# Optimization experiments

Measured on AMD Instinct MI355X. Metric: run time of the kernel, lower is better.

## Reference

```python
import jax, jax.numpy as jnp
from jax import lax
import numpy as np

HIDDEN = 256
UID_EMB, LOC_EMB, WD_EMB, HR_EMB = 64, 128, 16, 16
UID_NUM, LOC_NUM = 5000, 50000
S, L, C = 32, 32, 128   # steps, current-trace prefix length, candidates per step
HN, LH = 32, 64         # history traces, history trace length
EMB = UID_EMB + LOC_EMB + WD_EMB + HR_EMB  # 224


def setup_inputs() -> dict:
    key = jax.random.key(0)
    ks = jax.random.split(key, 20)
    def lin(k, o, i, s=0.05):
        return jax.random.normal(k, (o, i), jnp.float32) * s
    return {
        "uid": 7,
        "current_trace": jnp.stack([
            jax.random.randint(ks[0], (S, L), 0, LOC_NUM),
            jax.random.randint(ks[1], (S, L), 0, 7),
            jax.random.randint(ks[2], (S, L), 0, 24)], axis=-1),
        "history_trace": jnp.stack([
            jax.random.randint(ks[3], (HN, LH), 0, LOC_NUM),
            jax.random.randint(ks[4], (HN, LH), 0, 7),
            jax.random.randint(ks[5], (HN, LH), 0, 24)], axis=-1),
        "candidate_set": jax.random.randint(ks[6], (S, C), 0, LOC_NUM),
        "uid_emb": jax.random.normal(ks[7], (UID_NUM, UID_EMB), jnp.float32),
        "loc_emb": jax.random.normal(ks[8], (LOC_NUM, LOC_EMB), jnp.float32),
        "weekday_emb": jax.random.normal(ks[9], (7, WD_EMB), jnp.float32),
        "hour_emb": jax.random.normal(ks[10], (24, HR_EMB), jnp.float32),
        "W_ih": lin(ks[11], 3 * HIDDEN, EMB),
        "W_hh": lin(ks[12], 3 * HIDDEN, HIDDEN),
        "b_ih": jnp.zeros((3 * HIDDEN,), jnp.float32),
        "b_hh": jnp.zeros((3 * HIDDEN,), jnp.float32),
        "intra_w1": lin(ks[13], HIDDEN, HIDDEN),
        "intra_w2": lin(ks[14], HIDDEN, HIDDEN),
        "intra_out": lin(ks[15], 1, HIDDEN),
        "inter_w1": lin(ks[16], HIDDEN, HIDDEN),
        "inter_w2": lin(ks[17], HIDDEN, HIDDEN),
        "inter_out": lin(ks[18], 1, HIDDEN),
        "score_w": lin(ks[19], 1, HIDDEN),
    }


def _gru(x, W_ih, W_hh, b_ih, b_hh):
    # x: [B, T, D] -> all hidden states [B, T, H]; single-layer torch GRU equations
    B = x.shape[0]
    H = W_hh.shape[1]
    x_proj = x @ W_ih.T + b_ih  # [B, T, 3H], precomputed input projection
    def step(h, xp):
        gh = h @ W_hh.T + b_hh
        xr, xz, xn = jnp.split(xp, 3, axis=-1)
        hr, hz, hn = jnp.split(gh, 3, axis=-1)
        r = jax.nn.sigmoid(xr + hr)
        z = jax.nn.sigmoid(xz + hz)
        n = jnp.tanh(xn + r * hn)
        h_new = (1.0 - z) * n + z * h
        return h_new, h_new
    h0 = jnp.zeros((B, H), x.dtype)
    _, hs = lax.scan(step, h0, jnp.swapaxes(x_proj, 0, 1))
    return jnp.swapaxes(hs, 0, 1)


def _forward(uid, current_trace, history_trace, candidate_set,
             uid_emb, loc_emb, weekday_emb, hour_emb,
             W_ih, W_hh, b_ih, b_hh,
             intra_w1, intra_w2, intra_out,
             inter_w1, inter_w2, inter_out, score_w):
    def encode(trace):  # [B, T, 3] int -> [B, H]
        B, T, _ = trace.shape
        u = jnp.broadcast_to(uid_emb[uid][None, None, :], (B, T, UID_EMB))
        e = jnp.concatenate([u,
                             loc_emb[trace[:, :, 0]],
                             weekday_emb[trace[:, :, 1]],
                             hour_emb[trace[:, :, 2]]], axis=-1)
        hs = _gru(e, W_ih, W_hh, b_ih, b_hh)
        # intra-trajectory attention: query = last hidden state, key = all hidden states
        qh = jax.nn.relu(hs[:, -1, :] @ intra_w1.T)[:, None, :]
        kh = jax.nn.relu(hs @ intra_w2.T)
        a = (jnp.tanh(qh + kh) @ intra_out.T)[..., 0]  # [B, T]
        w = jax.nn.softmax(a, axis=1)
        return jnp.einsum('bt,bth->bh', w, hs)

    hist_hidden = encode(history_trace)  # [HN, H]

    S_, L_, _ = current_trace.shape
    C_ = candidate_set.shape[1]
    last_time = current_trace[:, -1, 1:3]  # [S, 2] weekday/hour of last observed point
    cand_point = jnp.concatenate(
        [candidate_set[..., None],
         jnp.broadcast_to(last_time[:, None, :], (S_, C_, 2))], axis=-1)  # [S, C, 3]
    cand_trace = jnp.concatenate(
        [jnp.broadcast_to(current_trace[:, None], (S_, C_, L_, 3)),
         cand_point[:, :, None, :]], axis=2)  # [S, C, L+1, 3]
    cand_hidden = encode(cand_trace.reshape(S_ * C_, L_ + 1, 3))  # [S*C, H]

    # inter-trajectory attention; history key is shared across all candidates
    qh = jax.nn.relu(cand_hidden @ inter_w1.T)      # [S*C, H]
    kh = jax.nn.relu(hist_hidden @ inter_w2.T)      # [HN, H]
    a = (jnp.tanh(qh[:, None, :] + kh[None]) @ inter_out.T)[..., 0]  # [S*C, HN]
    w = jax.nn.softmax(a, axis=1)
    moving = w @ hist_hidden                        # [S*C, H]

    scores = (moving @ score_w.T)[:, 0].reshape(S_, C_)
    probs = jax.nn.softmax(scores, axis=1)          # softmax over candidate set per step
    return probs, moving.reshape(S_, C_, HIDDEN)


def reference(uid, current_trace, history_trace, candidate_set,
              uid_emb, loc_emb, weekday_emb, hour_emb,
              W_ih, W_hh, b_ih, b_hh,
              intra_w1, intra_w2, intra_out,
              inter_w1, inter_w2, inter_out, score_w):
    return _forward(uid, current_trace, history_trace, candidate_set,
                    uid_emb, loc_emb, weekday_emb, hour_emb,
                    W_ih, W_hh, b_ih, b_hh,
                    intra_w1, intra_w2, intra_out,
                    inter_w1, inter_w2, inter_out, score_w)
```

## Files before the change

### kernel.cpp

```cpp
#include <hip/hip_runtime.h>
#include <math.h>

#define NHID   256
#define NEMB   224

constexpr int OFF_BASE = 0;
constexpr int OFF_WDP  = 768;
constexpr int OFF_HRP  = OFF_WDP + 7*768;
constexpr int OFF_XPH  = OFF_HRP + 24*768;
constexpr int OFF_XPC  = OFF_XPH + 32*64*768;
constexpr int OFF_HSH  = OFF_XPC + 32*32*768;
constexpr int OFF_HSC  = OFF_HSH + 32*64*256;
constexpr int OFF_GHL  = OFF_HSC + 32*32*256;
constexpr int OFF_QHH  = OFF_GHL + 32*768;
constexpr int OFF_HC   = OFF_QHH + 32*256;
constexpr int OFF_KHH  = OFF_HC  + 4096*256;
constexpr int OFF_KHSH = OFF_KHH + 32*64*256;
constexpr int OFF_KHC  = OFF_KHSH+ 32*32*256;
constexpr int OFF_QHC  = OFF_KHC + 4096*256;
constexpr int OFF_HIST = OFF_QHC + 4096*256;
constexpr int OFF_CHID = OFF_HIST+ 32*256;
constexpr int OFF_QH2  = OFF_CHID+ 4096*256;
constexpr int OFF_KH2  = OFF_QH2 + 4096*256;
constexpr int OFF_SC   = OFF_KH2 + 32*256;
constexpr int OFF_W16  = OFF_KHH;

__device__ __forceinline__ float sigm(float x) { return 1.0f / (1.0f + __expf(-x)); }
__device__ __forceinline__ float tanhf_fast(float x) {
  return 1.f - 2.f / (__expf(2.f * x) + 1.f);
}

typedef _Float16 half2_t __attribute__((ext_vector_type(2)));

__device__ __forceinline__ float fdot2f(unsigned int a, unsigned int b, float c) {
#if __has_builtin(__builtin_amdgcn_fdot2)
  return __builtin_amdgcn_fdot2(__builtin_bit_cast(half2_t, a),
                                __builtin_bit_cast(half2_t, b), c, false);
#else
  half2_t x = __builtin_bit_cast(half2_t, a);
  half2_t y = __builtin_bit_cast(half2_t, b);
  return c + (float)x[0] * (float)y[0] + (float)x[1] * (float)y[1];
#endif
}

__device__ __forceinline__ unsigned int packh(float a, float b) {
  unsigned short lo = __builtin_bit_cast(unsigned short, (_Float16)a);
  unsigned short hi = __builtin_bit_cast(unsigned short, (_Float16)b);
  return (unsigned int)lo | ((unsigned int)hi << 16);
}

__global__ __launch_bounds__(256) void k_prep(const int* uid, const float* uid_emb,
                                              const float* wde, const float* hre,
                                              const float* W_ih, const float* b_ih,
                                              const float* W_hh, float* ws) {
  __shared__ __align__(16) float ev[64];
  int blk = blockIdx.x, tid = threadIdx.x;
  if (blk >= 32) {
    int idx = (blk - 32) * 256 + tid;
    int i4 = idx & 31, j = idx >> 5;
    const float4* p = (const float4*)(W_hh + j * 256 + i4 * 8);
    float4 a = p[0], b = p[1];
    uint4 o;
    o.x = packh(a.x, a.y); o.y = packh(a.z, a.w);
    o.z = packh(b.x, b.y); o.w = packh(b.z, b.w);
    ((uint4*)((unsigned int*)ws + OFF_W16))[i4 * 768 + j] = o;
    return;
  }
  if (blk == 0) {
    if (tid < 64) ev[tid] = uid_emb[uid[0] * 64 + tid];
    __syncthreads();
    #pragma unroll
    for (int jj = 0; jj < 3; ++jj) {
      int j = tid + jj * 256;
      float acc = b_ih[j];
      const float* wr = W_ih + j * NEMB;
      #pragma unroll
      for (int k = 0; k < 64; k += 4) {
        float4 w = *(const float4*)(wr + k);
        acc += ev[k]*w.x + ev[k+1]*w.y + ev[k+2]*w.z + ev[k+3]*w.w;
      }
      ws[OFF_BASE + j] = acc;
    }
  } else if (blk < 8) {
    int wd = blk - 1;
    if (tid < 16) ev[tid] = wde[wd * 16 + tid];
    __syncthreads();
    #pragma unroll
    for (int jj = 0; jj < 3; ++jj) {
      int j = tid + jj * 256;
      float acc = 0.f;
      const float* wr = W_ih + j * NEMB + 192;
      #pragma unroll
      for (int k = 0; k < 16; k += 4) {
        float4 w = *(const float4*)(wr + k);
        acc += ev[k]*w.x + ev[k+1]*w.y + ev[k+2]*w.z + ev[k+3]*w.w;
      }
      ws[OFF_WDP + wd * 768 + j] = acc;
    }
  } else {
    int hr = blk - 8;
    if (tid < 16) ev[tid] = hre[hr * 16 + tid];
    __syncthreads();
    #pragma unroll
    for (int jj = 0; jj < 3; ++jj) {
      int j = tid + jj * 256;
      float acc = 0.f;
      const float* wr = W_ih + j * NEMB + 208;
      #pragma unroll
      for (int k = 0; k < 16; k += 4) {
        float4 w = *(const float4*)(wr + k);
        acc += ev[k]*w.x + ev[k+1]*w.y + ev[k+2]*w.z + ev[k+3]*w.w;
      }
      ws[OFF_HRP + hr * 768 + j] = acc;
    }
  }
}

__global__ __launch_bounds__(256) void k_xproj(const int* cur_tr, const int* hist_tr,
                                               const float* loc_emb, const float* W_ih,
                                               float* ws) {
  __shared__ float Ws[768][17];
  __shared__ float Xs[16][20];
  __shared__ int s_wd[16], s_hr[16], s_loc[16];
  int blk = blockIdx.x, tid = threadIdx.x;
  int r0 = blk * 16;

  if (tid < 16) {
    int row = r0 + tid;
    const int* tr; int idx;
    if (row < 2048) { tr = hist_tr; idx = row; } else { tr = cur_tr; idx = row - 2048; }
    s_loc[tid] = tr[idx * 3];
    s_wd[tid]  = tr[idx * 3 + 1];
    s_hr[tid]  = tr[idx * 3 + 2];
  }
  __syncthreads();

  float accA[16], accB[16], accC[16];
  #pragma unroll
  for (int r = 0; r < 16; ++r) { accA[r] = 0.f; accB[r] = 0.f; accC[r] = 0.f; }

  for (int kb = 0; kb < 8; ++kb) {
    for (int i = tid; i < 768 * 4; i += 256) {
      int j = i >> 2, q = (i & 3) * 4;
      float4 w = *(const float4*)&W_ih[j * NEMB + 64 + kb * 16 + q];
      Ws[j][q] = w.x; Ws[j][q+1] = w.y; Ws[j][q+2] = w.z; Ws[j][q+3] = w.w;
    }
    if (tid < 64) {
      int r = tid >> 2, q = (tid & 3) * 4;
      float4 x = *(const float4*)&loc_emb[s_loc[r] * 128 + kb * 16 + q];
      Xs[q][r] = x.x; Xs[q+1][r] = x.y; Xs[q+2][r] = x.z; Xs[q+3][r] = x.w;
    }
    __syncthreads();
    #pragma unroll
    for (int kk = 0; kk < 16; ++kk) {
      float wa = Ws[tid][kk], wb = Ws[tid + 256][kk], wc = Ws[tid + 512][kk];
      float4 x0 = *(const float4*)&Xs[kk][0];
      float4 x1 = *(const float4*)&Xs[kk][4];
      float4 x2 = *(const float4*)&Xs[kk][8];
      float4 x3 = *(const float4*)&Xs[kk][12];
      float xv[16] = {x0.x,x0.y,x0.z,x0.w, x1.x,x1.y,x1.z,x1.w,
                      x2.x,x2.y,x2.z,x2.w, x3.x,x3.y,x3.z,x3.w};
      #pragma unroll
      for (int r = 0; r < 16; ++r) {
        accA[r] += xv[r] * wa; accB[r] += xv[r] * wb; accC[r] += xv[r] * wc;
      }
    }
    __syncthreads();
  }

  float bA = ws[OFF_BASE + tid], bB = ws[OFF_BASE + 256 + tid], bC = ws[OFF_BASE + 512 + tid];
  for (int r = 0; r < 16; ++r) {
    int row = r0 + r;
    float* outp = (row < 2048) ? (ws + OFF_XPH + row * 768)
                               : (ws + OFF_XPC + (row - 2048) * 768);
    const float* wdp = ws + OFF_WDP + s_wd[r] * 768;
    const float* hrp = ws + OFF_HRP + s_hr[r] * 768;
    outp[tid]       = accA[r] + bA + wdp[tid]       + hrp[tid];
    outp[256 + tid] = accB[r] + bB + wdp[256 + tid] + hrp[256 + tid];
    outp[512 + tid] = accC[r] + bC + wdp[512 + tid] + hrp[512 + tid];
  }
}

__global__ __launch_bounds__(768) void k_gru(const float* b_hh, const float* intra_w1,
                                             float* ws) {
  __shared__ __align__(16) float gh[768];
  __shared__ __align__(16) float h32[256];
  __shared__ __align__(16) unsigned short h16[256];
  int w = blockIdx.x, tid = threadIdx.x;
  int T; const float* xp; float* hs;
  if (w < 32) { T = 64; xp = ws + OFF_XPH + w * 64 * 768; hs = ws + OFF_HSH + w * 64 * 256; }
  else        { T = 32; int b = w - 32; xp = ws + OFF_XPC + b * 32 * 768; hs = ws + OFF_HSC + b * 32 * 256; }

  uint4 wreg[32];
  {
    const uint4* wp = (const uint4*)((const unsigned int*)ws + OFF_W16) + tid;
    #pragma unroll
    for (int i = 0; i < 32; ++i) wreg[i] = wp[i * 768];
  }
  float bh = b_hh[tid];
  if (tid < 256) { h32[tid] = 0.f; h16[tid] = 0; }
  __syncthreads();

  for (int t = 0; t < T; ++t) {
    float xr, xz, xn;
    if (tid < 256) {
      xr = xp[t * 768 + tid];
      xz = xp[t * 768 + 256 + tid];
      xn = xp[t * 768 + 512 + tid];
    }
    float acc = bh;
    const uint4* hp = (const uint4*)h16;
    #pragma unroll
    for (int i = 0; i < 32; ++i) {
      uint4 hv = hp[i];
      acc = fdot2f(wreg[i].x, hv.x, acc);
      acc = fdot2f(wreg[i].y, hv.y, acc);
      acc = fdot2f(wreg[i].z, hv.z, acc);
      acc = fdot2f(wreg[i].w, hv.w, acc);
    }
    gh[tid] = acc;
    __syncthreads();
    if (tid < 256) {
      float r  = sigm(xr + gh[tid]);
      float z  = sigm(xz + gh[256 + tid]);
      float n  = tanhf_fast(xn + r * gh[512 + tid]);
      float hn = (1.f - z) * n + z * h32[tid];
      h32[tid] = hn;
      hs[t * 256 + tid] = hn;
      h16[tid] = __builtin_bit_cast(unsigned short, (_Float16)hn);
    }
    __syncthreads();
  }

  if (w < 32) {
    if (tid < 256) {
      float acc = 0.f;
      const float* r1 = intra_w1 + tid * 256;
      #pragma unroll 16
      for (int k = 0; k < 256; k += 4) {
        float4 wv = *(const float4*)(r1 + k);
        float4 hv = *(const float4*)&h32[k];
        acc += hv.x*wv.x + hv.y*wv.y + hv.z*wv.z + hv.w*wv.w;
      }
      ws[OFF_QHH + w * 256 + tid] = fmaxf(acc, 0.f);
    }
  } else {
    float acc = bh;
    const uint4* hp = (const uint4*)h16;
    #pragma unroll
    for (int i = 0; i < 32; ++i) {
      uint4 hv = hp[i];
      acc = fdot2f(wreg[i].x, hv.x, acc);
      acc = fdot2f(wreg[i].y, hv.y, acc);
      acc = fdot2f(wreg[i].z, hv.z, acc);
      acc = fdot2f(wreg[i].w, hv.w, acc);
    }
    ws[OFF_GHL + (w - 32) * 768 + tid] = acc;
  }
}

__global__ __launch_bounds__(256) void k_cand(const int* cur_tr, const int* cand_set,
                                              const float* loc_emb, const float* W_ih,
                                              float* ws) {
  __shared__ float Ws[768][17];
  __shared__ float Xs[16][20];
  int blk = blockIdx.x, tid = threadIdx.x;
  int r0 = blk * 16;
  int s = r0 >> 7;

  float accA[16], accB[16], accC[16];
  #pragma unroll
  for (int r = 0; r < 16; ++r) { accA[r] = 0.f; accB[r] = 0.f; accC[r] = 0.f; }

  for (int kb = 0; kb < 8; ++kb) {
    for (int i = tid; i < 768 * 4; i += 256) {
      int j = i >> 2, q = (i & 3) * 4;
      float4 w = *(const float4*)&W_ih[j * NEMB + 64 + kb * 16 + q];
      Ws[j][q] = w.x; Ws[j][q+1] = w.y; Ws[j][q+2] = w.z; Ws[j][q+3] = w.w;
    }
    if (tid < 64) {
      int r = tid >> 2, q = (tid & 3) * 4;
      float4 x = *(const float4*)&loc_emb[cand_set[r0 + r] * 128 + kb * 16 + q];
      Xs[q][r] = x.x; Xs[q+1][r] = x.y; Xs[q+2][r] = x.z; Xs[q+3][r] = x.w;
    }
    __syncthreads();
    #pragma unroll
    for (int kk = 0; kk < 16; ++kk) {
      float wa = Ws[tid][kk], wb = Ws[tid + 256][kk], wc = Ws[tid + 512][kk];
      float4 x0 = *(const float4*)&Xs[kk][0];
      float4 x1 = *(const float4*)&Xs[kk][4];
      float4 x2 = *(const float4*)&Xs[kk][8];
      float4 x3 = *(const float4*)&Xs[kk][12];
      float xv[16] = {x0.x,x0.y,x0.z,x0.w, x1.x,x1.y,x1.z,x1.w,
                      x2.x,x2.y,x2.z,x2.w, x3.x,x3.y,x3.z,x3.w};
      #pragma unroll
      for (int r = 0; r < 16; ++r) {
        accA[r] += xv[r] * wa; accB[r] += xv[r] * wb; accC[r] += xv[r] * wc;
      }
    }
    __syncthreads();
  }

  int last = s * 32 + 31;
  int wd = cur_tr[last * 3 + 1], hr = cur_tr[last * 3 + 2];
  const float* wdp = ws + OFF_WDP + wd * 768;
  const float* hrp = ws + OFF_HRP + hr * 768;
  float xbA = ws[OFF_BASE + tid]       + wdp[tid]       + hrp[tid];
  float xbB = ws[OFF_BASE + 256 + tid] + wdp[256 + tid] + hrp[256 + tid];
  float xbC = ws[OFF_BASE + 512 + tid] + wdp[512 + tid] + hrp[512 + tid];
  float ghr = ws[OFF_GHL + s * 768 + tid];
  float ghz = ws[OFF_GHL + s * 768 + 256 + tid];
  float ghn = ws[OFF_GHL + s * 768 + 512 + tid];
  float hp  = ws[OFF_HSC + last * 256 + tid];

  for (int r = 0; r < 16; ++r) {
    float rr = sigm(xbA + accA[r] + ghr);
    float zz = sigm(xbB + accB[r] + ghz);
    float nn = tanhf_fast(xbC + accC[r] + ghn);
    float hn = (1.f - zz) * nn + zz * hp;
    ws[OFF_HC + (r0 + r) * 256 + tid] = hn;
  }
}

__device__ __forceinline__ void proj_body(const float* in, float* out, const float* W,
                                          int r0, int tid) {
  __shared__ float Ws[256][33];
  __shared__ float Xs[32][36];
  int c0 = tid & 63, rg = (tid >> 6) * 8;
  float acc[4][8];
  #pragma unroll
  for (int c = 0; c < 4; ++c)
    #pragma unroll
    for (int r = 0; r < 8; ++r) acc[c][r] = 0.f;

  for (int kb = 0; kb < 8; ++kb) {
    for (int i = tid; i < 256 * 8; i += 256) {
      int j = i >> 3, q = (i & 7) * 4;
      float4 v = *(const float4*)&W[j * 256 + kb * 32 + q];
      Ws[j][q] = v.x; Ws[j][q+1] = v.y; Ws[j][q+2] = v.z; Ws[j][q+3] = v.w;
    }
    {
      int r = tid >> 3, q = (tid & 7) * 4;
      float4 v = *(const float4*)&in[(r0 + r) * 256 + kb * 32 + q];
      Xs[q][r] = v.x; Xs[q+1][r] = v.y; Xs[q+2][r] = v.z; Xs[q+3][r] = v.w;
    }
    __syncthreads();
    #pragma unroll
    for (int kk = 0; kk < 32; ++kk) {
      float w0 = Ws[c0][kk], w1 = Ws[c0 + 64][kk], w2 = Ws[c0 + 128][kk], w3 = Ws[c0 + 192][kk];
      float4 xa = *(const float4*)&Xs[kk][rg];
      float4 xb = *(const float4*)&Xs[kk][rg + 4];
      float xv[8] = {xa.x,xa.y,xa.z,xa.w, xb.x,xb.y,xb.z,xb.w};
      #pragma unroll
      for (int r = 0; r < 8; ++r) {
        acc[0][r] += xv[r] * w0; acc[1][r] += xv[r] * w1;
        acc[2][r] += xv[r] * w2; acc[3][r] += xv[r] * w3;
      }
    }
    __syncthreads();
  }
  #pragma unroll
  for (int c = 0; c < 4; ++c)
    for (int r = 0; r < 8; ++r)
      out[(r0 + rg + r) * 256 + c0 + c * 64] = fmaxf(acc[c][r], 0.f);
}

__global__ __launch_bounds__(256) void k_proj_intra(const float* intra_w1, const float* intra_w2,
                                                    float* ws) {
  int blk = blockIdx.x, tid = threadIdx.x;
  const float* in; float* out; const float* W; int r0;
  if (blk < 64)       { in = ws + OFF_HSH; out = ws + OFF_KHH;  W = intra_w2; r0 = blk * 32; }
  else if (blk < 96)  { in = ws + OFF_HSC; out = ws + OFF_KHSH; W = intra_w2; r0 = (blk - 64) * 32; }
  else if (blk < 224) { in = ws + OFF_HC;  out = ws + OFF_KHC;  W = intra_w2; r0 = (blk - 96) * 32; }
  else                { in = ws + OFF_HC;  out = ws + OFF_QHC;  W = intra_w1; r0 = (blk - 224) * 32; }
  proj_body(in, out, W, r0, tid);
}

__global__ __launch_bounds__(256) void k_proj_inter(const float* inter_w1, const float* inter_w2,
                                                    float* ws) {
  int blk = blockIdx.x, tid = threadIdx.x;
  const float* in; float* out; const float* W; int r0;
  if (blk < 128) { in = ws + OFF_CHID; out = ws + OFF_QH2; W = inter_w1; r0 = blk * 32; }
  else           { in = ws + OFF_HIST; out = ws + OFF_KH2; W = inter_w2; r0 = 0; }
  proj_body(in, out, W, r0, tid);
}

__global__ __launch_bounds__(256) void k_hist_attn(const float* intra_out, float* ws) {
  __shared__ __align__(16) float a[64];
  int b = blockIdx.x, tid = threadIdx.x;
  int wv = tid >> 6, lane = tid & 63;
  const float* qh = ws + OFF_QHH + b * 256;
  const float* kh = ws + OFF_KHH + b * 64 * 256;
  const float* hs = ws + OFF_HSH + b * 64 * 256;

  float4 q4  = *(const float4*)&qh[lane * 4];
  float4 io4 = *(const float4*)&intra_out[lane * 4];
  for (int t = wv; t < 64; t += 4) {
    float4 k4 = *(const float4*)&kh[t * 256 + lane * 4];
    float p = tanhf_fast(q4.x + k4.x) * io4.x + tanhf_fast(q4.y + k4.y) * io4.y +
              tanhf_fast(q4.z + k4.z) * io4.z + tanhf_fast(q4.w + k4.w) * io4.w;
    #pragma unroll
    for (int off = 32; off; off >>= 1) p += __shfl_down(p, off);
    if (lane == 0) a[t] = p;
  }
  __syncthreads();
  if (tid < 64) {
    float v = a[tid];
    float m = v;
    #pragma unroll
    for (int off = 32; off; off >>= 1) m = fmaxf(m, __shfl_xor(m, off));
    float e = __expf(v - m);
    float ssum = e;
    #pragma unroll
    for (int off = 32; off; off >>= 1) ssum += __shfl_xor(ssum, off);
    a[tid] = e / ssum;
  }
  __syncthreads();
  float acc = 0.f;
  for (int t = 0; t < 64; ++t) acc += a[t] * hs[t * 256 + tid];
  ws[OFF_HIST + b * 256 + tid] = acc;
}

__global__ __launch_bounds__(256) void k_cand_attn(const float* intra_out, float* ws) {
  __shared__ float Ks[32][260];
  __shared__ float Kc[4][260];
  __shared__ float Qs[4][260];
  __shared__ float Io[260];
  __shared__ float aw[4][36];
  int blk = blockIdx.x, tid = threadIdx.x;
  int s = blk >> 5;
  int bId0 = s * 128 + (blk & 31) * 4;
  int w = tid >> 6, lane = tid & 63;

  for (int i = tid; i < 32 * 256; i += 256) {
    int t = i >> 8, d = i & 255;
    Ks[t][d] = ws[OFF_KHSH + (s * 32 + t) * 256 + d];
  }
  for (int i = tid; i < 4 * 256; i += 256) {
    int c = i >> 8, d = i & 255;
    Kc[c][d] = ws[OFF_KHC + (bId0 + c) * 256 + d];
    Qs[c][d] = ws[OFF_QHC + (bId0 + c) * 256 + d];
  }
  Io[tid] = intra_out[tid];
  __syncthreads();

  const float* krow = (lane < 32) ? &Ks[lane][0] : &Kc[w][0];
  float p = 0.f;
  for (int d = 0; d < 256; d += 4) {
    float4 k4 = *(const float4*)&krow[d];
    float4 q4 = *(const float4*)&Qs[w][d];
    float4 i4 = *(const float4*)&Io[d];
    p += tanhf_fast(q4.x + k4.x) * i4.x + tanhf_fast(q4.y + k4.y) * i4.y +
         tanhf_fast(q4.z + k4.z) * i4.z + tanhf_fast(q4.w + k4.w) * i4.w;
  }
  if (lane >= 33) p = -1e30f;
  float m = p;
  #pragma unroll
  for (int off = 32; off; off >>= 1) m = fmaxf(m, __shfl_xor(m, off));
  float e = __expf(p - m);
  float ssum = e;
  #pragma unroll
  for (int off = 32; off; off >>= 1) ssum += __shfl_xor(ssum, off);
  float wt = e / ssum;
  if (lane < 33) aw[w][lane] = wt;
  __syncthreads();

  const float* hsc = ws + OFF_HSC + s * 32 * 256;
  const float* hc  = ws + OFF_HC + (bId0 + w) * 256;
  float ax = 0.f, ay = 0.f, az = 0.f, az2 = 0.f;
  for (int t = 0; t < 32; ++t) {
    float wt2 = aw[w][t];
    float4 hv = *(const float4*)&hsc[t * 256 + lane * 4];
    ax += wt2 * hv.x; ay += wt2 * hv.y; az += wt2 * hv.z; az2 += wt2 * hv.w;
  }
  {
    float wt2 = aw[w][32];
    float4 hv = *(const float4*)&hc[lane * 4];
    ax += wt2 * hv.x; ay += wt2 * hv.y; az += wt2 * hv.z; az2 += wt2 * hv.w;
  }
  float4 o; o.x = ax; o.y = ay; o.z = az; o.w = az2;
  *(float4*)&ws[OFF_CHID + (bId0 + w) * 256 + lane * 4] = o;
}

__global__ __launch_bounds__(256) void k_inter_attn(const float* inter_out, const float* score_w,
                                                    float* ws, float* d_out) {
  __shared__ float Ks[32][260];
  __shared__ float Qs[4][260];
  __shared__ float Io[260];
  __shared__ float aw[4][36];
  int blk = blockIdx.x, tid = threadIdx.x;
  int bId0 = blk * 4;
  int w = tid >> 6, lane = tid & 63;

  for (int i = tid; i < 32 * 256; i += 256) {
    int t = i >> 8, d = i & 255;
    Ks[t][d] = ws[OFF_KH2 + t * 256 + d];
  }
  for (int i = tid; i < 4 * 256; i += 256) {
    int c = i >> 8, d = i & 255;
    Qs[c][d] = ws[OFF_QH2 + (bId0 + c) * 256 + d];
  }
  Io[tid] = inter_out[tid];
  __syncthreads();

  const float* krow = (lane < 32) ? &Ks[lane][0] : &Ks[0][0];
  float p = 0.f;
  for (int d = 0; d < 256; d += 4) {
    float4 k4 = *(const float4*)&krow[d];
    float4 q4 = *(const float4*)&Qs[w][d];
    float4 i4 = *(const float4*)&Io[d];
    p += tanhf_fast(q4.x + k4.x) * i4.x + tanhf_fast(q4.y + k4.y) * i4.y +
         tanhf_fast(q4.z + k4.z) * i4.z + tanhf_fast(q4.w + k4.w) * i4.w;
  }
  if (lane >= 32) p = -1e30f;
  float m = p;
  #pragma unroll
  for (int off = 32; off; off >>= 1) m = fmaxf(m, __shfl_xor(m, off));
  float e = __expf(p - m);
  float ssum = e;
  #pragma unroll
  for (int off = 32; off; off >>= 1) ssum += __shfl_xor(ssum, off);
  float wt = e / ssum;
  if (lane < 32) aw[w][lane] = wt;
  __syncthreads();

  const float* hist = ws + OFF_HIST;
  float ax = 0.f, ay = 0.f, az = 0.f, az2 = 0.f;
  for (int t = 0; t < 32; ++t) {
    float wt2 = aw[w][t];
    float4 hv = *(const float4*)&hist[t * 256 + lane * 4];
    ax += wt2 * hv.x; ay += wt2 * hv.y; az += wt2 * hv.z; az2 += wt2 * hv.w;
  }
  float4 o; o.x = ax; o.y = ay; o.z = az; o.w = az2;
  *(float4*)&d_out[4096 + (bId0 + w) * 256 + lane * 4] = o;
  float4 sw = *(const float4*)&score_w[lane * 4];
  float sc = ax*sw.x + ay*sw.y + az*sw.z + az2*sw.w;
  #pragma unroll
  for (int off = 32; off; off >>= 1) sc += __shfl_xor(sc, off);
  if (lane == 0) ws[OFF_SC + bId0 + w] = sc;
}

__global__ __launch_bounds__(64) void k_probs(const float* ws, float* d_out) {
  int s = blockIdx.x, lane = threadIdx.x;
  float v0 = ws[OFF_SC + s * 128 + lane];
  float v1 = ws[OFF_SC + s * 128 + 64 + lane];
  float m = fmaxf(v0, v1);
  #pragma unroll
  for (int off = 32; off; off >>= 1) m = fmaxf(m, __shfl_xor(m, off));
  float e0 = __expf(v0 - m), e1 = __expf(v1 - m);
  float ssum = e0 + e1;
  #pragma unroll
  for (int off = 32; off; off >>= 1) ssum += __shfl_xor(ssum, off);
  float inv = 1.f / ssum;
  d_out[s * 128 + lane] = e0 * inv;
  d_out[s * 128 + 64 + lane] = e1 * inv;
}

extern "C" void kernel_launch(void* const* d_in, const int* in_sizes, int n_in,
                              void* d_out, int out_size, void* d_ws, size_t ws_size,
                              hipStream_t stream) {
  const int*   uid      = (const int*)  d_in[0];
  const int*   cur_tr   = (const int*)  d_in[1];
  const int*   hist_tr  = (const int*)  d_in[2];
  const int*   cand_set = (const int*)  d_in[3];
  const float* uid_emb  = (const float*)d_in[4];
  const float* loc_emb  = (const float*)d_in[5];
  const float* wde      = (const float*)d_in[6];
  const float* hre      = (const float*)d_in[7];
  const float* W_ih     = (const float*)d_in[8];
  const float* W_hh     = (const float*)d_in[9];
  const float* b_ih     = (const float*)d_in[10];
  const float* b_hh     = (const float*)d_in[11];
  const float* intra_w1 = (const float*)d_in[12];
  const float* intra_w2 = (const float*)d_in[13];
  const float* intra_out= (const float*)d_in[14];
  const float* inter_w1 = (const float*)d_in[15];
  const float* inter_w2 = (const float*)d_in[16];
  const float* inter_out= (const float*)d_in[17];
  const float* score_w  = (const float*)d_in[18];
  float* ws  = (float*)d_ws;
  float* out = (float*)d_out;

  hipLaunchKernelGGL(k_prep,       dim3(128),  dim3(256), 0, stream, uid, uid_emb, wde, hre, W_ih, b_ih, W_hh, ws);
  hipLaunchKernelGGL(k_xproj,      dim3(192),  dim3(256), 0, stream, cur_tr, hist_tr, loc_emb, W_ih, ws);
  hipLaunchKernelGGL(k_gru,        dim3(64),   dim3(768), 0, stream, b_hh, intra_w1, ws);
  hipLaunchKernelGGL(k_cand,       dim3(256),  dim3(256), 0, stream, cur_tr, cand_set, loc_emb, W_ih, ws);
  hipLaunchKernelGGL(k_proj_intra, dim3(352),  dim3(256), 0, stream, intra_w1, intra_w2, ws);
  hipLaunchKernelGGL(k_hist_attn,  dim3(32),   dim3(256), 0, stream, intra_out, ws);
  hipLaunchKernelGGL(k_cand_attn,  dim3(1024), dim3(256), 0, stream, intra_out, ws);
  hipLaunchKernelGGL(k_proj_inter, dim3(129),  dim3(256), 0, stream, inter_w1, inter_w2, ws);
  hipLaunchKernelGGL(k_inter_attn, dim3(1024), dim3(256), 0, stream, inter_out, score_w, ws, out);
  hipLaunchKernelGGL(k_probs,      dim3(32),   dim3(64),  0, stream, ws, out);
}
```

Baseline: 440.5 us.

## Fuse inter projections into attention kernels and use packed fp16 dot products

The intra projection now packs weights and activations to half pairs and accumulates with a two-wide dot instruction, halving shared-memory footprint and FMA count. The inter_w2 projection of the history vectors moves into k_hist_attn. The inter_w1 projection is fused into a new k_inter_pipe kernel that handles 8 candidates per block, which removes one launch and the QH2 round trip through global memory. In exchange, each inter block re-reads the full inter_w1 from global or L2 and the projections run at reduced precision.

```diff
diff --git a/kernel.cpp b/kernel.cpp
--- a/kernel.cpp
+++ b/kernel.cpp
@@ -322,10 +322,10 @@
   }
 }
 
-__device__ __forceinline__ void proj_body(const float* in, float* out, const float* W,
-                                          int r0, int tid) {
-  __shared__ float Ws[256][33];
-  __shared__ float Xs[32][36];
+__device__ __forceinline__ void proj_body16(const float* in, float* out, const float* W,
+                                            int r0, int tid) {
+  __shared__ unsigned int WsH[256][21];
+  __shared__ unsigned int XsH[16][40];
   int c0 = tid & 63, rg = (tid >> 6) * 8;
   float acc[4][8];
   #pragma unroll
@@ -335,26 +335,31 @@
 
   for (int kb = 0; kb < 8; ++kb) {
     for (int i = tid; i < 256 * 8; i += 256) {
-      int j = i >> 3, q = (i & 7) * 4;
-      float4 v = *(const float4*)&W[j * 256 + kb * 32 + q];
-      Ws[j][q] = v.x; Ws[j][q+1] = v.y; Ws[j][q+2] = v.z; Ws[j][q+3] = v.w;
+      int j = i >> 3, q = i & 7;
+      float4 v = *(const float4*)&W[j * 256 + kb * 32 + q * 4];
+      WsH[j][q * 2]     = packh(v.x, v.y);
+      WsH[j][q * 2 + 1] = packh(v.z, v.w);
     }
     {
-      int r = tid >> 3, q = (tid & 7) * 4;
-      float4 v = *(const float4*)&in[(r0 + r) * 256 + kb * 32 + q];
-      Xs[q][r] = v.x; Xs[q+1][r] = v.y; Xs[q+2][r] = v.z; Xs[q+3][r] = v.w;
-    }
-    __syncthreads();
-    #pragma unroll
-    for (int kk = 0; kk < 32; ++kk) {
-      float w0 = Ws[c0][kk], w1 = Ws[c0 + 64][kk], w2 = Ws[c0 + 128][kk], w3 = Ws[c0 + 192][kk];
-      float4 xa = *(const float4*)&Xs[kk][rg];
-      float4 xb = *(const float4*)&Xs[kk][rg + 4];
-      float xv[8] = {xa.x,xa.y,xa.z,xa.w, xb.x,xb.y,xb.z,xb.w};
+      int r = tid >> 3, q = tid & 7;
+      float4 v = *(const float4*)&in[(r0 + r) * 256 + kb * 32 + q * 4];
+      XsH[q * 2][r]     = packh(v.x, v.y);
+      XsH[q * 2 + 1][r] = packh(v.z, v.w);
+    }
+    __syncthreads();
+    #pragma unroll
+    for (int kk = 0; kk < 16; ++kk) {
+      unsigned int w0 = WsH[c0][kk],       w1 = WsH[c0 + 64][kk];
+      unsigned int w2 = WsH[c0 + 128][kk], w3 = WsH[c0 + 192][kk];
+      uint4 xa = *(const uint4*)&XsH[kk][rg];
+      uint4 xb = *(const uint4*)&XsH[kk][rg + 4];
+      unsigned int xv[8] = {xa.x, xa.y, xa.z, xa.w, xb.x, xb.y, xb.z, xb.w};
       #pragma unroll
       for (int r = 0; r < 8; ++r) {
-        acc[0][r] += xv[r] * w0; acc[1][r] += xv[r] * w1;
-        acc[2][r] += xv[r] * w2; acc[3][r] += xv[r] * w3;
+        acc[0][r] = fdot2f(w0, xv[r], acc[0][r]);
+        acc[1][r] = fdot2f(w1, xv[r], acc[1][r]);
+        acc[2][r] = fdot2f(w2, xv[r], acc[2][r]);
+        acc[3][r] = fdot2f(w3, xv[r], acc[3][r]);
       }
     }
     __syncthreads();
@@ -373,20 +378,13 @@
   else if (blk < 96)  { in = ws + OFF_HSC; out = ws + OFF_KHSH; W = intra_w2; r0 = (blk - 64) * 32; }
   else if (blk < 224) { in = ws + OFF_HC;  out = ws + OFF_KHC;  W = intra_w2; r0 = (blk - 96) * 32; }
   else                { in = ws + OFF_HC;  out = ws + OFF_QHC;  W = intra_w1; r0 = (blk - 224) * 32; }
-  proj_body(in, out, W, r0, tid);
-}
-
-__global__ __launch_bounds__(256) void k_proj_inter(const float* inter_w1, const float* inter_w2,
-                                                    float* ws) {
-  int blk = blockIdx.x, tid = threadIdx.x;
-  const float* in; float* out; const float* W; int r0;
-  if (blk < 128) { in = ws + OFF_CHID; out = ws + OFF_QH2; W = inter_w1; r0 = blk * 32; }
-  else           { in = ws + OFF_HIST; out = ws + OFF_KH2; W = inter_w2; r0 = 0; }
-  proj_body(in, out, W, r0, tid);
-}
-
-__global__ __launch_bounds__(256) void k_hist_attn(const float* intra_out, float* ws) {
+  proj_body16(in, out, W, r0, tid);
+}
+
+__global__ __launch_bounds__(256) void k_hist_attn(const float* intra_out, const float* inter_w2,
+                                                   float* ws) {
   __shared__ __align__(16) float a[64];
+  __shared__ __align__(16) float hrow[260];
   int b = blockIdx.x, tid = threadIdx.x;
   int wv = tid >> 6, lane = tid & 63;
   const float* qh = ws + OFF_QHH + b * 256;
@@ -419,6 +417,17 @@
   float acc = 0.f;
   for (int t = 0; t < 64; ++t) acc += a[t] * hs[t * 256 + tid];
   ws[OFF_HIST + b * 256 + tid] = acc;
+  hrow[tid] = acc;
+  __syncthreads();
+  float acck = 0.f;
+  const float* w2r = inter_w2 + tid * 256;
+  #pragma unroll 8
+  for (int k = 0; k < 256; k += 4) {
+    float4 wv2 = *(const float4*)(w2r + k);
+    float4 hv  = *(const float4*)&hrow[k];
+    acck += hv.x*wv2.x + hv.y*wv2.y + hv.z*wv2.z + hv.w*wv2.w;
+  }
+  ws[OFF_KH2 + b * 256 + tid] = fmaxf(acck, 0.f);
 }
 
 __global__ __launch_bounds__(256) void k_cand_attn(const float* intra_out, float* ws) {
@@ -482,62 +491,95 @@
   *(float4*)&ws[OFF_CHID + (bId0 + w) * 256 + lane * 4] = o;
 }
 
-__global__ __launch_bounds__(256) void k_inter_attn(const float* inter_out, const float* score_w,
-                                                    float* ws, float* d_out) {
+__global__ __launch_bounds__(256) void k_inter_pipe(const float* inter_w1, const float* inter_out,
+                                                    const float* score_w, float* ws, float* d_out) {
   __shared__ float Ks[32][260];
-  __shared__ float Qs[4][260];
+  __shared__ float Hs[32][260];
+  __shared__ unsigned int ctdh[128][12];
+  __shared__ float qh2s[8][260];
   __shared__ float Io[260];
-  __shared__ float aw[4][36];
+  __shared__ float aw[8][36];
   int blk = blockIdx.x, tid = threadIdx.x;
-  int bId0 = blk * 4;
+  int bId0 = blk * 8;
   int w = tid >> 6, lane = tid & 63;
 
   for (int i = tid; i < 32 * 256; i += 256) {
     int t = i >> 8, d = i & 255;
     Ks[t][d] = ws[OFF_KH2 + t * 256 + d];
-  }
-  for (int i = tid; i < 4 * 256; i += 256) {
-    int c = i >> 8, d = i & 255;
-    Qs[c][d] = ws[OFF_QH2 + (bId0 + c) * 256 + d];
+    Hs[t][d] = ws[OFF_HIST + t * 256 + d];
+  }
+  for (int i = tid; i < 8 * 128; i += 256) {
+    int c = i >> 7, k2 = i & 127;
+    float2 v = *(const float2*)&ws[OFF_CHID + (bId0 + c) * 256 + k2 * 2];
+    ctdh[k2][c] = packh(v.x, v.y);
   }
   Io[tid] = inter_out[tid];
   __syncthreads();
 
-  const float* krow = (lane < 32) ? &Ks[lane][0] : &Ks[0][0];
-  float p = 0.f;
-  for (int d = 0; d < 256; d += 4) {
-    float4 k4 = *(const float4*)&krow[d];
-    float4 q4 = *(const float4*)&Qs[w][d];
-    float4 i4 = *(const float4*)&Io[d];
-    p += tanhf_fast(q4.x + k4.x) * i4.x + tanhf_fast(q4.y + k4.y) * i4.y +
-         tanhf_fast(q4.z + k4.z) * i4.z + tanhf_fast(q4.w + k4.w) * i4.w;
-  }
-  if (lane >= 32) p = -1e30f;
-  float m = p;
-  #pragma unroll
-  for (int off = 32; off; off >>= 1) m = fmaxf(m, __shfl_xor(m, off));
-  float e = __expf(p - m);
-  float ssum = e;
-  #pragma unroll
-  for (int off = 32; off; off >>= 1) ssum += __shfl_xor(ssum, off);
-  float wt = e / ssum;
-  if (lane < 32) aw[w][lane] = wt;
-  __syncthreads();
-
-  const float* hist = ws + OFF_HIST;
-  float ax = 0.f, ay = 0.f, az = 0.f, az2 = 0.f;
-  for (int t = 0; t < 32; ++t) {
-    float wt2 = aw[w][t];
-    float4 hv = *(const float4*)&hist[t * 256 + lane * 4];
-    ax += wt2 * hv.x; ay += wt2 * hv.y; az += wt2 * hv.z; az2 += wt2 * hv.w;
-  }
-  float4 o; o.x = ax; o.y = ay; o.z = az; o.w = az2;
-  *(float4*)&d_out[4096 + (bId0 + w) * 256 + lane * 4] = o;
+  float acc[8];
+  #pragma unroll
+  for (int c = 0; c < 8; ++c) acc[c] = 0.f;
+  const float* wr = inter_w1 + tid * 256;
+  for (int k = 0; k < 256; k += 4) {
+    float4 wv = *(const float4*)(wr + k);
+    unsigned int w01 = packh(wv.x, wv.y), w23 = packh(wv.z, wv.w);
+    int k2 = k >> 1;
+    uint4 xa = *(const uint4*)&ctdh[k2][0];
+    uint4 xb = *(const uint4*)&ctdh[k2][4];
+    uint4 xc = *(const uint4*)&ctdh[k2 + 1][0];
+    uint4 xd = *(const uint4*)&ctdh[k2 + 1][4];
+    acc[0] = fdot2f(w01, xa.x, acc[0]); acc[0] = fdot2f(w23, xc.x, acc[0]);
+    acc[1] = fdot2f(w01, xa.y, acc[1]); acc[1] = fdot2f(w23, xc.y, acc[1]);
+    acc[2] = fdot2f(w01, xa.z, acc[2]); acc[2] = fdot2f(w23, xc.z, acc[2]);
+    acc[3] = fdot2f(w01, xa.w, acc[3]); acc[3] = fdot2f(w23, xc.w, acc[3]);
+    acc[4] = fdot2f(w01, xb.x, acc[4]); acc[4] = fdot2f(w23, xd.x, acc[4]);
+    acc[5] = fdot2f(w01, xb.y, acc[5]); acc[5] = fdot2f(w23, xd.y, acc[5]);
+    acc[6] = fdot2f(w01, xb.z, acc[6]); acc[6] = fdot2f(w23, xd.z, acc[6]);
+    acc[7] = fdot2f(w01, xb.w, acc[7]); acc[7] = fdot2f(w23, xd.w, acc[7]);
+  }
+  #pragma unroll
+  for (int c = 0; c < 8; ++c) qh2s[c][tid] = fmaxf(acc[c], 0.f);
+  __syncthreads();
+
+  {
+    int c = (lane < 32) ? w : (w + 4);
+    int t = lane & 31;
+    float p = 0.f;
+    for (int d = 0; d < 256; d += 4) {
+      float4 k4 = *(const float4*)&Ks[t][d];
+      float4 q4 = *(const float4*)&qh2s[c][d];
+      float4 i4 = *(const float4*)&Io[d];
+      p += tanhf_fast(q4.x + k4.x) * i4.x + tanhf_fast(q4.y + k4.y) * i4.y +
+           tanhf_fast(q4.z + k4.z) * i4.z + tanhf_fast(q4.w + k4.w) * i4.w;
+    }
+    float m = p;
+    #pragma unroll
+    for (int off = 16; off; off >>= 1) m = fmaxf(m, __shfl_xor(m, off, 32));
+    float e = __expf(p - m);
+    float ssum = e;
+    #pragma unroll
+    for (int off = 16; off; off >>= 1) ssum += __shfl_xor(ssum, off, 32);
+    aw[c][t] = e / ssum;
+  }
+  __syncthreads();
+
   float4 sw = *(const float4*)&score_w[lane * 4];
-  float sc = ax*sw.x + ay*sw.y + az*sw.z + az2*sw.w;
-  #pragma unroll
-  for (int off = 32; off; off >>= 1) sc += __shfl_xor(sc, off);
-  if (lane == 0) ws[OFF_SC + bId0 + w] = sc;
+  #pragma unroll
+  for (int cc = 0; cc < 2; ++cc) {
+    int c = w + cc * 4;
+    float ax = 0.f, ay = 0.f, az = 0.f, az2 = 0.f;
+    for (int t = 0; t < 32; ++t) {
+      float wt2 = aw[c][t];
+      float4 hv = *(const float4*)&Hs[t][lane * 4];
+      ax += wt2 * hv.x; ay += wt2 * hv.y; az += wt2 * hv.z; az2 += wt2 * hv.w;
+    }
+    float4 o; o.x = ax; o.y = ay; o.z = az; o.w = az2;
+    *(float4*)&d_out[4096 + (bId0 + c) * 256 + lane * 4] = o;
+    float sc = ax*sw.x + ay*sw.y + az*sw.z + az2*sw.w;
+    #pragma unroll
+    for (int off = 32; off; off >>= 1) sc += __shfl_xor(sc, off);
+    if (lane == 0) ws[OFF_SC + bId0 + c] = sc;
+  }
 }
 
 __global__ __launch_bounds__(64) void k_probs(const float* ws, float* d_out) {
@@ -586,9 +628,8 @@
   hipLaunchKernelGGL(k_gru,        dim3(64),   dim3(768), 0, stream, b_hh, intra_w1, ws);
   hipLaunchKernelGGL(k_cand,       dim3(256),  dim3(256), 0, stream, cur_tr, cand_set, loc_emb, W_ih, ws);
   hipLaunchKernelGGL(k_proj_intra, dim3(352),  dim3(256), 0, stream, intra_w1, intra_w2, ws);
-  hipLaunchKernelGGL(k_hist_attn,  dim3(32),   dim3(256), 0, stream, intra_out, ws);
+  hipLaunchKernelGGL(k_hist_attn,  dim3(32),   dim3(256), 0, stream, intra_out, inter_w2, ws);
   hipLaunchKernelGGL(k_cand_attn,  dim3(1024), dim3(256), 0, stream, intra_out, ws);
-  hipLaunchKernelGGL(k_proj_inter, dim3(129),  dim3(256), 0, stream, inter_w1, inter_w2, ws);
-  hipLaunchKernelGGL(k_inter_attn, dim3(1024), dim3(256), 0, stream, inter_out, score_w, ws, out);
+  hipLaunchKernelGGL(k_inter_pipe, dim3(512),  dim3(256), 0, stream, inter_w1, inter_out, score_w, ws, out);
   hipLaunchKernelGGL(k_probs,      dim3(32),   dim3(64),  0, stream, ws, out);
 }
```

After: 426.7 us. 1.03x faster.
